# Performance work log

Hardware: AMD Instinct MI355X
Metric: run time of the kernel (lower is better)

The kernel has to match this reference:

```python
import jax, jax.numpy as jnp
import numpy as np

B, S, DIM = 4, 2048, 512
HEADS, DHEAD = 8, 64
INNER = HEADS * DHEAD


def setup_inputs() -> dict:
    key = jax.random.key(0)
    k1, k2, k3, k4 = jax.random.split(key, 4)
    x = jax.random.normal(k1, (B, S, DIM), dtype=jnp.float32)
    W_qkv = jax.random.normal(k2, (DIM, 3 * INNER), dtype=jnp.float32) * (DIM ** -0.5)
    W_out = jax.random.normal(k3, (INNER, DIM), dtype=jnp.float32) * (INNER ** -0.5)
    b_out = jnp.zeros((DIM,), dtype=jnp.float32)
    # learnable log-temperature, initialized to log(dim_head**-0.5)
    log_temp = jnp.asarray(np.log(DHEAD ** -0.5), dtype=jnp.float32)
    return {"x": x, "W_qkv": W_qkv, "log_temp": log_temp, "W_out": W_out, "b_out": b_out}


def reference(x, W_qkv, log_temp, W_out, b_out):
    b, s, _ = x.shape
    qkv = x @ W_qkv  # [b, s, 3*inner]
    q, k, v = jnp.split(qkv, 3, axis=-1)
    # [b, s, inner] -> [b, h, s, d]
    reshape = lambda t: t.reshape(b, s, HEADS, DHEAD).transpose(0, 2, 1, 3)
    q, k, v = reshape(q), reshape(k), reshape(v)
    dots = jnp.einsum("bhid,bhjd->bhij", q, k) * jnp.exp(log_temp)
    mask_value = -jnp.finfo(dots.dtype).max
    eye = jnp.eye(s, dtype=bool)
    dots = jnp.where(eye, mask_value, dots)
    attn = jax.nn.softmax(dots, axis=-1)
    out = jnp.einsum("bhij,bhjd->bhid", attn, v)
    out = out.transpose(0, 2, 1, 3).reshape(b, s, INNER)
    return out @ W_out + b_out
```

## Files before the change

kernel.cpp:

```cpp
#include <hip/hip_runtime.h>
#include <hip/hip_bf16.h>

#define BB 4
#define SS 2048
#define DIMM 512
#define HH 8
#define DD 64
#define NQKV 1536

typedef float  floatx4 __attribute__((ext_vector_type(4)));
typedef short  bf16x8  __attribute__((ext_vector_type(8)));
typedef short  bf16x4  __attribute__((ext_vector_type(4)));

#define MFMA16(A, B, C) __builtin_amdgcn_mfma_f32_16x16x32_bf16(A, B, C, 0, 0, 0)

__device__ __forceinline__ floatx4 MFMA16K16(bf16x4 a, bf16x4 b, floatx4 c) {
#if __has_builtin(__builtin_amdgcn_mfma_f32_16x16x16bf16_1k)
    return __builtin_amdgcn_mfma_f32_16x16x16bf16_1k(a, b, c, 0, 0, 0);
#else
    floatx4 d;
    asm volatile("v_mfma_f32_16x16x16_bf16 %0, %1, %2, %3"
                 : "=v"(d) : "v"(a), "v"(b), "v"(c));
    return d;
#endif
}

__device__ __forceinline__ unsigned short f2bf(float f) {
    unsigned int u = __float_as_uint(f);
    u += 0x7FFFu + ((u >> 16) & 1u);
    return (unsigned short)(u >> 16);
}

__device__ __forceinline__ unsigned int f2bf_pk(float lo, float hi) {
    float2 f; f.x = lo; f.y = hi;
    __hip_bfloat162 h = __float22bfloat162_rn(f);
    return *reinterpret_cast<unsigned int*>(&h);
}

__device__ __forceinline__ float fast_exp2(float x) {
#if __has_builtin(__builtin_amdgcn_exp2f)
    return __builtin_amdgcn_exp2f(x);
#else
    return __exp2f(x);
#endif
}

__device__ __forceinline__ void gl_lds16(const void* g, void* l) {
    __builtin_amdgcn_global_load_lds(
        (__attribute__((address_space(1))) void*)g,
        (__attribute__((address_space(3))) void*)l,
        16, 0, 0);
}

__global__ __launch_bounds__(256) void k_prep(
    const float* __restrict__ x, const float* __restrict__ W_qkv,
    const float* __restrict__ W_out,
    unsigned short* __restrict__ xb, unsigned short* __restrict__ Wq_t,
    unsigned short* __restrict__ Wo_t) {
    __shared__ float t[32][33];
    int bid = blockIdx.x, tid = threadIdx.x;
    if (bid < 4096) {
        int i = (bid * 256 + tid) * 4;
        float4 v = *(const float4*)(x + i);
        ushort4 o;
        o.x = f2bf(v.x); o.y = f2bf(v.y); o.z = f2bf(v.z); o.w = f2bf(v.w);
        *(ushort4*)(xb + i) = o;
        return;
    }
    const float* in; unsigned short* out; int R = 512, C, bx, by;
    if (bid < 4864) { in = W_qkv; out = Wq_t; C = 1536; int blk = bid - 4096; bx = blk % 48; by = blk / 48; }
    else            { in = W_out; out = Wo_t; C = 512;  int blk = bid - 4864; bx = blk % 16; by = blk / 16; }
    int tx = tid & 31, ty = tid >> 5;
    int c0 = bx * 32, r0 = by * 32;
    for (int i = 0; i < 4; i++) {
        int r = r0 + ty + i * 8;
        t[ty + i * 8][tx] = in[(size_t)r * C + c0 + tx];
    }
    __syncthreads();
    for (int i = 0; i < 4; i++) {
        int cc = c0 + ty + i * 8;
        out[(size_t)cc * R + r0 + tx] = f2bf(t[tx][ty + i * 8]);
    }
}

__global__ __launch_bounds__(256) void k_gemm_qkv(
    const unsigned short* __restrict__ A,
    const unsigned short* __restrict__ Bt,
    const float* __restrict__ log_temp,
    unsigned short* __restrict__ Qb,
    unsigned short* __restrict__ Kb,
    unsigned short* __restrict__ Vt) {
    __shared__ unsigned short smem[2][128 * 64];
    unsigned short* As = smem[0];
    unsigned short* Bs = smem[1];
    const int K = 512;
    int m0 = blockIdx.x * 128, n0 = blockIdx.y * 128;
    int tid = threadIdx.x;
    int w = tid >> 6, lane = tid & 63;
    int c = lane & 15, q4 = lane >> 4;
    int wm = w >> 1, wn = w & 1;
    float qscale = __expf(log_temp[0]) * 1.44269504f;

    floatx4 acc[4][4] = {};

    for (int k0 = 0; k0 < K; k0 += 64) {
        __syncthreads();
        for (int i = 0; i < 4; i++) {
            int cidx = w * 256 + i * 64 + lane;
            int row = cidx >> 3, cc = cidx & 7;
            int gcc = cc ^ (row & 7);
            gl_lds16(A + (size_t)(m0 + row) * K + k0 + gcc * 8,
                     As + (size_t)(w * 256 + i * 64) * 8);
            gl_lds16(Bt + (size_t)(n0 + row) * K + k0 + gcc * 8,
                     Bs + (size_t)(w * 256 + i * 64) * 8);
        }
        __syncthreads();
        bf16x8 aF[2][4], bF[2][4];
        for (int kh = 0; kh < 2; kh++)
            for (int mt = 0; mt < 4; mt++) {
                int row = wm * 64 + mt * 16 + c;
                aF[kh][mt] = *(const bf16x8*)&As[row * 64 + (((kh * 4 + q4) ^ (row & 7)) * 8)];
            }
        for (int kh = 0; kh < 2; kh++)
            for (int nt = 0; nt < 4; nt++) {
                int row = wn * 64 + nt * 16 + c;
                bF[kh][nt] = *(const bf16x8*)&Bs[row * 64 + (((kh * 4 + q4) ^ (row & 7)) * 8)];
            }
        for (int kh = 0; kh < 2; kh++)
            for (int mt = 0; mt < 4; mt++)
                for (int nt = 0; nt < 4; nt++)
                    acc[mt][nt] = MFMA16(aF[kh][mt], bF[kh][nt], acc[mt][nt]);
    }

    if (n0 < 1024) {
        for (int nt = 0; nt < 4; nt++) {
            int n = n0 + wn * 64 + nt * 16 + c;
            int t = n >> 9, inner = n & 511;
            int h = inner >> 6, d = inner & 63;
            for (int mt = 0; mt < 4; mt++) {
                for (int r = 0; r < 4; r++) {
                    int m = m0 + wm * 64 + mt * 16 + q4 * 4 + r;
                    int b = m >> 11, s = m & 2047;
                    int bh = b * 8 + h;
                    float v = acc[mt][nt][r];
                    if (t == 0)  Qb[((size_t)bh * SS + s) * 64 + d] = f2bf(v * qscale);
                    else         Kb[((size_t)bh * SS + s) * 64 + d] = f2bf(v);
                }
            }
        }
    } else {
        unsigned short* T = &smem[0][0];
        int b = m0 >> 11, s_base = m0 & 2047;
        for (int half = 0; half < 2; half++) {
            __syncthreads();
            if (wn == half) {
                for (int nt = 0; nt < 4; nt++)
                    for (int mt = 0; mt < 4; mt++)
                        for (int r = 0; r < 4; r++)
                            T[(nt * 16 + c) * 136 + wm * 64 + mt * 16 + q4 * 4 + r] =
                                f2bf(acc[mt][nt][r]);
            }
            __syncthreads();
            for (int rr = 0; rr < 4; rr++) {
                int nl = w * 16 + rr * 4 + q4;
                int ml = c * 8;
                bf16x8 v = *(const bf16x8*)&T[nl * 136 + ml];
                int n = n0 + half * 64 + nl;
                int h = (n >> 6) - 16, d = n & 63;
                int bh = b * 8 + h;
                *(bf16x8*)(Vt + ((size_t)bh * 64 + d) * SS + s_base + ml) = v;
            }
        }
    }
}

__global__ __launch_bounds__(256, 4) void k_attn(
    const unsigned short* __restrict__ Qb,
    const unsigned short* __restrict__ Kb,
    const unsigned short* __restrict__ Vt,
    unsigned short* __restrict__ AO) {
    __shared__ unsigned short Ks[2][64 * 64];
    __shared__ unsigned short Vs[2][64 * 64];
    int q0 = blockIdx.x * 128;
    int h = blockIdx.y, b = blockIdx.z;
    int bh = b * 8 + h;
    int tid = threadIdx.x, w = tid >> 6, lane = tid & 63;
    int c = lane & 15, q4 = lane >> 4;

    const unsigned short* Kbase = Kb + (size_t)bh * SS * 64;
    const unsigned short* Vbase = Vt + (size_t)bh * 64 * SS;

    bf16x8 qf[2][2];
    for (int mi = 0; mi < 2; mi++) {
        const unsigned short* qp = Qb + ((size_t)bh * SS + q0 + w * 32 + mi * 16 + c) * 64;
        qf[mi][0] = *(const bf16x8*)(qp + q4 * 8);
        qf[mi][1] = *(const bf16x8*)(qp + 32 + q4 * 8);
    }

    const unsigned short* ksrc[2];
    const unsigned short* vsrc[2];
    for (int i = 0; i < 2; i++) {
        int cidx = i * 256 + tid;
        int grow = cidx >> 3, gcc = (cidx & 7) ^ (grow & 7);
        ksrc[i] = Kbase + (size_t)grow * 64 + gcc * 8;
        vsrc[i] = Vbase + (size_t)grow * SS + gcc * 8;
    }

    for (int i = 0; i < 2; i++) {
        gl_lds16(ksrc[i], Ks[0] + (i * 256 + w * 64) * 8);
        gl_lds16(vsrc[i], Vs[0] + (i * 256 + w * 64) * 8);
    }

    int mask_j0 = (q0 + w * 32) & ~63;
    int mglob0 = q0 + w * 32 + c;
    int mglob1 = mglob0 + 16;
    floatx4 oacc[2][4] = {};
    float psum0 = 0.f, psum1 = 0.f;

    for (int j0 = 0; j0 < SS; j0 += 64) {
        int buf = (j0 >> 6) & 1;
        __syncthreads();
        if (j0 + 64 < SS) {
            for (int i = 0; i < 2; i++) {
                gl_lds16(ksrc[i] + (size_t)(j0 + 64) * 64, Ks[buf ^ 1] + (i * 256 + w * 64) * 8);
                gl_lds16(vsrc[i] + (j0 + 64), Vs[buf ^ 1] + (i * 256 + w * 64) * 8);
            }
        }
        bool diag = (j0 == mask_j0);

        for (int jt = 0; jt < 4; jt++) {
            int row = jt * 16 + c;
            bf16x8 kf0 = *(const bf16x8*)&Ks[buf][row * 64 + ((q4 ^ (row & 7)) * 8)];
            bf16x8 kf1 = *(const bf16x8*)&Ks[buf][row * 64 + (((4 + q4) ^ (row & 7)) * 8)];
            floatx4 sa0 = {}, sa1 = {};
            sa0 = MFMA16(kf0, qf[0][0], sa0);
            sa0 = MFMA16(kf1, qf[0][1], sa0);
            sa1 = MFMA16(kf0, qf[1][0], sa1);
            sa1 = MFMA16(kf1, qf[1][1], sa1);

            if (diag) {
                for (int r = 0; r < 4; r++) {
                    int jg = j0 + jt * 16 + q4 * 4 + r;
                    if (jg == mglob0) sa0[r] = -1e30f;
                    if (jg == mglob1) sa1[r] = -1e30f;
                }
            }

            float e0 = fast_exp2(sa0[0]), e1 = fast_exp2(sa0[1]);
            float e2 = fast_exp2(sa0[2]), e3 = fast_exp2(sa0[3]);
            psum0 += (e0 + e1) + (e2 + e3);
            union { bf16x4 v; unsigned int u[2]; } P0;
            P0.u[0] = f2bf_pk(e0, e1); P0.u[1] = f2bf_pk(e2, e3);
            float f0 = fast_exp2(sa1[0]), f1 = fast_exp2(sa1[1]);
            float f2 = fast_exp2(sa1[2]), f3 = fast_exp2(sa1[3]);
            psum1 += (f0 + f1) + (f2 + f3);
            union { bf16x4 v; unsigned int u[2]; } P1;
            P1.u[0] = f2bf_pk(f0, f1); P1.u[1] = f2bf_pk(f2, f3);

            int chunk = jt * 2 + (q4 >> 1);
            int sub = (q4 & 1) * 4;
            for (int dt = 0; dt < 4; dt++) {
                int vrow = dt * 16 + c;
                bf16x4 vf = *(const bf16x4*)&Vs[buf][vrow * 64 + ((chunk ^ (vrow & 7)) * 8) + sub];
                oacc[0][dt] = MFMA16K16(P0.v, vf, oacc[0][dt]);
                oacc[1][dt] = MFMA16K16(P1.v, vf, oacc[1][dt]);
            }
        }
    }

    for (int mi = 0; mi < 2; mi++) {
        float l = (mi == 0) ? psum0 : psum1;
        l += __shfl_xor(l, 16);
        l += __shfl_xor(l, 32);
        for (int r = 0; r < 4; r++) {
            float lr = __shfl(l, q4 * 4 + r, 64);
            float inv = 1.0f / lr;
            int s = q0 + w * 32 + mi * 16 + q4 * 4 + r;
            for (int dt = 0; dt < 4; dt++)
                AO[((size_t)b * SS + s) * 512 + h * 64 + dt * 16 + c] =
                    f2bf(oacc[mi][dt][r] * inv);
        }
    }
}

__global__ __launch_bounds__(256) void k_gemm_out(
    const unsigned short* __restrict__ A,
    const unsigned short* __restrict__ Bt,
    const float* __restrict__ bias,
    float* __restrict__ out) {
    __shared__ unsigned short As[128 * 64];
    __shared__ unsigned short Bs[128 * 64];
    const int K = 512;
    int m0 = blockIdx.x * 128, n0 = blockIdx.y * 128;
    int tid = threadIdx.x;
    int w = tid >> 6, lane = tid & 63;
    int c = lane & 15, q4 = lane >> 4;
    int wm = w >> 1, wn = w & 1;

    floatx4 acc[4][4] = {};

    for (int k0 = 0; k0 < K; k0 += 64) {
        __syncthreads();
        for (int i = 0; i < 4; i++) {
            int cidx = w * 256 + i * 64 + lane;
            int row = cidx >> 3, cc = cidx & 7;
            int gcc = cc ^ (row & 7);
            gl_lds16(A + (size_t)(m0 + row) * K + k0 + gcc * 8,
                     As + (size_t)(w * 256 + i * 64) * 8);
            gl_lds16(Bt + (size_t)(n0 + row) * K + k0 + gcc * 8,
                     Bs + (size_t)(w * 256 + i * 64) * 8);
        }
        __syncthreads();
        bf16x8 aF[2][4], bF[2][4];
        for (int kh = 0; kh < 2; kh++)
            for (int mt = 0; mt < 4; mt++) {
                int row = wm * 64 + mt * 16 + c;
                aF[kh][mt] = *(const bf16x8*)&As[row * 64 + (((kh * 4 + q4) ^ (row & 7)) * 8)];
            }
        for (int kh = 0; kh < 2; kh++)
            for (int nt = 0; nt < 4; nt++) {
                int row = wn * 64 + nt * 16 + c;
                bF[kh][nt] = *(const bf16x8*)&Bs[row * 64 + (((kh * 4 + q4) ^ (row & 7)) * 8)];
            }
        for (int kh = 0; kh < 2; kh++)
            for (int mt = 0; mt < 4; mt++)
                for (int nt = 0; nt < 4; nt++)
                    acc[mt][nt] = MFMA16(aF[kh][mt], bF[kh][nt], acc[mt][nt]);
    }

    for (int nt = 0; nt < 4; nt++) {
        int n = n0 + wn * 64 + nt * 16 + c;
        float bv = bias[n];
        for (int mt = 0; mt < 4; mt++) {
            for (int r = 0; r < 4; r++) {
                int m = m0 + wm * 64 + mt * 16 + q4 * 4 + r;
                out[(size_t)m * 512 + n] = acc[mt][nt][r] + bv;
            }
        }
    }
}

extern "C" void kernel_launch(void* const* d_in, const int* in_sizes, int n_in,
                              void* d_out, int out_size, void* d_ws, size_t ws_size,
                              hipStream_t stream) {
    const float* x        = (const float*)d_in[0];
    const float* W_qkv    = (const float*)d_in[1];
    const float* log_temp = (const float*)d_in[2];
    const float* W_out    = (const float*)d_in[3];
    const float* b_out    = (const float*)d_in[4];
    float* out = (float*)d_out;

    char* ws = (char*)d_ws;
    unsigned short* xb   = (unsigned short*)(ws + 0);
    unsigned short* Wq_t = (unsigned short*)(ws + 8388608);
    unsigned short* Wo_t = (unsigned short*)(ws + 9961472);
    unsigned short* Qb   = (unsigned short*)(ws + 10485760);
    unsigned short* Kb   = (unsigned short*)(ws + 18874368);
    unsigned short* Vt   = (unsigned short*)(ws + 27262976);
    unsigned short* AO   = (unsigned short*)(ws + 35651584);

    k_prep<<<5120, 256, 0, stream>>>(x, W_qkv, W_out, xb, Wq_t, Wo_t);
    k_gemm_qkv<<<dim3(64, 12), 256, 0, stream>>>(xb, Wq_t, log_temp, Qb, Kb, Vt);
    k_attn<<<dim3(16, 8, 4), 256, 0, stream>>>(Qb, Kb, Vt, AO);
    k_gemm_out<<<dim3(64, 4), 256, 0, stream>>>(AO, Wo_t, b_out, out);
}
```

Baseline: 167.9 us.

## Split attention rows across 8 waves and halve output GEMM M-tile

The attention kernel now runs 512 threads per block, and each wave owns 16 query rows instead of 32. Each thread issues a single K/V staging load per tile, so more waves share each K/V tile in LDS and latency hiding improves. The output projection GEMM switches to 64x128 tiles with one 16-row strip per wave, doubling the grid to 512 blocks to fill more CUs. The cost is less register reuse per wave, since each K fragment now feeds only one Q tile, and more B-tile traffic per output.

New measurement: 164.6 us. 1.02x faster.

```diff
diff --git a/kernel.cpp b/kernel.cpp
--- a/kernel.cpp
+++ b/kernel.cpp
@@ -174,7 +174,7 @@
     }
 }
 
-__global__ __launch_bounds__(256, 4) void k_attn(
+__global__ __launch_bounds__(512, 4) void k_attn(
     const unsigned short* __restrict__ Qb,
     const unsigned short* __restrict__ Kb,
     const unsigned short* __restrict__ Vt,
@@ -190,41 +190,33 @@
     const unsigned short* Kbase = Kb + (size_t)bh * SS * 64;
     const unsigned short* Vbase = Vt + (size_t)bh * 64 * SS;
 
-    bf16x8 qf[2][2];
-    for (int mi = 0; mi < 2; mi++) {
-        const unsigned short* qp = Qb + ((size_t)bh * SS + q0 + w * 32 + mi * 16 + c) * 64;
-        qf[mi][0] = *(const bf16x8*)(qp + q4 * 8);
-        qf[mi][1] = *(const bf16x8*)(qp + 32 + q4 * 8);
-    }
-
-    const unsigned short* ksrc[2];
-    const unsigned short* vsrc[2];
-    for (int i = 0; i < 2; i++) {
-        int cidx = i * 256 + tid;
-        int grow = cidx >> 3, gcc = (cidx & 7) ^ (grow & 7);
-        ksrc[i] = Kbase + (size_t)grow * 64 + gcc * 8;
-        vsrc[i] = Vbase + (size_t)grow * SS + gcc * 8;
-    }
-
-    for (int i = 0; i < 2; i++) {
-        gl_lds16(ksrc[i], Ks[0] + (i * 256 + w * 64) * 8);
-        gl_lds16(vsrc[i], Vs[0] + (i * 256 + w * 64) * 8);
-    }
-
-    int mask_j0 = (q0 + w * 32) & ~63;
-    int mglob0 = q0 + w * 32 + c;
-    int mglob1 = mglob0 + 16;
-    floatx4 oacc[2][4] = {};
-    float psum0 = 0.f, psum1 = 0.f;
+    bf16x8 qf[2];
+    {
+        const unsigned short* qp = Qb + ((size_t)bh * SS + q0 + w * 16 + c) * 64;
+        qf[0] = *(const bf16x8*)(qp + q4 * 8);
+        qf[1] = *(const bf16x8*)(qp + 32 + q4 * 8);
+    }
+
+    int grow = tid >> 3, gcc = (tid & 7) ^ (grow & 7);
+    const unsigned short* ksrc = Kbase + (size_t)grow * 64 + gcc * 8;
+    const unsigned short* vsrc = Vbase + (size_t)grow * SS + gcc * 8;
+    unsigned short* kdst = (unsigned short*)Ks[0] + w * 512;
+    unsigned short* vdst = (unsigned short*)Vs[0] + w * 512;
+
+    gl_lds16(ksrc, kdst);
+    gl_lds16(vsrc, vdst);
+
+    int mask_j0 = (q0 + w * 16) & ~63;
+    int mglob = q0 + w * 16 + c;
+    floatx4 oacc[4] = {};
+    float psum = 0.f;
 
     for (int j0 = 0; j0 < SS; j0 += 64) {
         int buf = (j0 >> 6) & 1;
         __syncthreads();
         if (j0 + 64 < SS) {
-            for (int i = 0; i < 2; i++) {
-                gl_lds16(ksrc[i] + (size_t)(j0 + 64) * 64, Ks[buf ^ 1] + (i * 256 + w * 64) * 8);
-                gl_lds16(vsrc[i] + (j0 + 64), Vs[buf ^ 1] + (i * 256 + w * 64) * 8);
-            }
+            gl_lds16(ksrc + (size_t)(j0 + 64) * 64, kdst + (buf ^ 1) * 4096);
+            gl_lds16(vsrc + (j0 + 64), vdst + (buf ^ 1) * 4096);
         }
         bool diag = (j0 == mask_j0);
 
@@ -232,54 +224,43 @@
             int row = jt * 16 + c;
             bf16x8 kf0 = *(const bf16x8*)&Ks[buf][row * 64 + ((q4 ^ (row & 7)) * 8)];
             bf16x8 kf1 = *(const bf16x8*)&Ks[buf][row * 64 + (((4 + q4) ^ (row & 7)) * 8)];
-            floatx4 sa0 = {}, sa1 = {};
-            sa0 = MFMA16(kf0, qf[0][0], sa0);
-            sa0 = MFMA16(kf1, qf[0][1], sa0);
-            sa1 = MFMA16(kf0, qf[1][0], sa1);
-            sa1 = MFMA16(kf1, qf[1][1], sa1);
+            floatx4 sa = {};
+            sa = MFMA16(kf0, qf[0], sa);
+            sa = MFMA16(kf1, qf[1], sa);
 
             if (diag) {
                 for (int r = 0; r < 4; r++) {
                     int jg = j0 + jt * 16 + q4 * 4 + r;
-                    if (jg == mglob0) sa0[r] = -1e30f;
-                    if (jg == mglob1) sa1[r] = -1e30f;
+                    if (jg == mglob) sa[r] = -1e30f;
                 }
             }
 
-            float e0 = fast_exp2(sa0[0]), e1 = fast_exp2(sa0[1]);
-            float e2 = fast_exp2(sa0[2]), e3 = fast_exp2(sa0[3]);
-            psum0 += (e0 + e1) + (e2 + e3);
-            union { bf16x4 v; unsigned int u[2]; } P0;
-            P0.u[0] = f2bf_pk(e0, e1); P0.u[1] = f2bf_pk(e2, e3);
-            float f0 = fast_exp2(sa1[0]), f1 = fast_exp2(sa1[1]);
-            float f2 = fast_exp2(sa1[2]), f3 = fast_exp2(sa1[3]);
-            psum1 += (f0 + f1) + (f2 + f3);
-            union { bf16x4 v; unsigned int u[2]; } P1;
-            P1.u[0] = f2bf_pk(f0, f1); P1.u[1] = f2bf_pk(f2, f3);
+            float e0 = fast_exp2(sa[0]), e1 = fast_exp2(sa[1]);
+            float e2 = fast_exp2(sa[2]), e3 = fast_exp2(sa[3]);
+            psum += (e0 + e1) + (e2 + e3);
+            union { bf16x4 v; unsigned int u[2]; } P;
+            P.u[0] = f2bf_pk(e0, e1); P.u[1] = f2bf_pk(e2, e3);
 
             int chunk = jt * 2 + (q4 >> 1);
             int sub = (q4 & 1) * 4;
             for (int dt = 0; dt < 4; dt++) {
                 int vrow = dt * 16 + c;
                 bf16x4 vf = *(const bf16x4*)&Vs[buf][vrow * 64 + ((chunk ^ (vrow & 7)) * 8) + sub];
-                oacc[0][dt] = MFMA16K16(P0.v, vf, oacc[0][dt]);
-                oacc[1][dt] = MFMA16K16(P1.v, vf, oacc[1][dt]);
-            }
-        }
-    }
-
-    for (int mi = 0; mi < 2; mi++) {
-        float l = (mi == 0) ? psum0 : psum1;
-        l += __shfl_xor(l, 16);
-        l += __shfl_xor(l, 32);
-        for (int r = 0; r < 4; r++) {
-            float lr = __shfl(l, q4 * 4 + r, 64);
-            float inv = 1.0f / lr;
-            int s = q0 + w * 32 + mi * 16 + q4 * 4 + r;
-            for (int dt = 0; dt < 4; dt++)
-                AO[((size_t)b * SS + s) * 512 + h * 64 + dt * 16 + c] =
-                    f2bf(oacc[mi][dt][r] * inv);
-        }
+                oacc[dt] = MFMA16K16(P.v, vf, oacc[dt]);
+            }
+        }
+    }
+
+    float l = psum;
+    l += __shfl_xor(l, 16);
+    l += __shfl_xor(l, 32);
+    for (int r = 0; r < 4; r++) {
+        float lr = __shfl(l, q4 * 4 + r, 64);
+        float inv = 1.0f / lr;
+        int s = q0 + w * 16 + q4 * 4 + r;
+        for (int dt = 0; dt < 4; dt++)
+            AO[((size_t)b * SS + s) * 512 + h * 64 + dt * 16 + c] =
+                f2bf(oacc[dt][r] * inv);
     }
 }
 
@@ -288,54 +269,54 @@
     const unsigned short* __restrict__ Bt,
     const float* __restrict__ bias,
     float* __restrict__ out) {
-    __shared__ unsigned short As[128 * 64];
+    __shared__ unsigned short As[64 * 64];
     __shared__ unsigned short Bs[128 * 64];
     const int K = 512;
-    int m0 = blockIdx.x * 128, n0 = blockIdx.y * 128;
+    int m0 = blockIdx.x * 64, n0 = blockIdx.y * 128;
     int tid = threadIdx.x;
     int w = tid >> 6, lane = tid & 63;
     int c = lane & 15, q4 = lane >> 4;
-    int wm = w >> 1, wn = w & 1;
-
-    floatx4 acc[4][4] = {};
+
+    floatx4 acc[8] = {};
 
     for (int k0 = 0; k0 < K; k0 += 64) {
         __syncthreads();
-        for (int i = 0; i < 4; i++) {
-            int cidx = w * 256 + i * 64 + lane;
+        for (int i = 0; i < 2; i++) {
+            int cidx = i * 256 + tid;
             int row = cidx >> 3, cc = cidx & 7;
             int gcc = cc ^ (row & 7);
             gl_lds16(A + (size_t)(m0 + row) * K + k0 + gcc * 8,
-                     As + (size_t)(w * 256 + i * 64) * 8);
+                     As + (size_t)(i * 256 + w * 64) * 8);
+        }
+        for (int i = 0; i < 4; i++) {
+            int cidx = i * 256 + tid;
+            int row = cidx >> 3, cc = cidx & 7;
+            int gcc = cc ^ (row & 7);
             gl_lds16(Bt + (size_t)(n0 + row) * K + k0 + gcc * 8,
-                     Bs + (size_t)(w * 256 + i * 64) * 8);
-        }
-        __syncthreads();
-        bf16x8 aF[2][4], bF[2][4];
-        for (int kh = 0; kh < 2; kh++)
-            for (int mt = 0; mt < 4; mt++) {
-                int row = wm * 64 + mt * 16 + c;
-                aF[kh][mt] = *(const bf16x8*)&As[row * 64 + (((kh * 4 + q4) ^ (row & 7)) * 8)];
-            }
-        for (int kh = 0; kh < 2; kh++)
-            for (int nt = 0; nt < 4; nt++) {
-                int row = wn * 64 + nt * 16 + c;
+                     Bs + (size_t)(i * 256 + w * 64) * 8);
+        }
+        __syncthreads();
+        bf16x8 aF[2], bF[2][8];
+        for (int kh = 0; kh < 2; kh++) {
+            int row = w * 16 + c;
+            aF[kh] = *(const bf16x8*)&As[row * 64 + (((kh * 4 + q4) ^ (row & 7)) * 8)];
+        }
+        for (int kh = 0; kh < 2; kh++)
+            for (int nt = 0; nt < 8; nt++) {
+                int row = nt * 16 + c;
                 bF[kh][nt] = *(const bf16x8*)&Bs[row * 64 + (((kh * 4 + q4) ^ (row & 7)) * 8)];
             }
         for (int kh = 0; kh < 2; kh++)
-            for (int mt = 0; mt < 4; mt++)
-                for (int nt = 0; nt < 4; nt++)
-                    acc[mt][nt] = MFMA16(aF[kh][mt], bF[kh][nt], acc[mt][nt]);
-    }
-
-    for (int nt = 0; nt < 4; nt++) {
-        int n = n0 + wn * 64 + nt * 16 + c;
+            for (int nt = 0; nt < 8; nt++)
+                acc[nt] = MFMA16(aF[kh], bF[kh][nt], acc[nt]);
+    }
+
+    for (int nt = 0; nt < 8; nt++) {
+        int n = n0 + nt * 16 + c;
         float bv = bias[n];
-        for (int mt = 0; mt < 4; mt++) {
-            for (int r = 0; r < 4; r++) {
-                int m = m0 + wm * 64 + mt * 16 + q4 * 4 + r;
-                out[(size_t)m * 512 + n] = acc[mt][nt][r] + bv;
-            }
+        for (int r = 0; r < 4; r++) {
+            int m = m0 + w * 16 + q4 * 4 + r;
+            out[(size_t)m * 512 + n] = acc[nt][r] + bv;
         }
     }
 }
@@ -361,6 +342,6 @@
 
     k_prep<<<5120, 256, 0, stream>>>(x, W_qkv, W_out, xb, Wq_t, Wo_t);
     k_gemm_qkv<<<dim3(64, 12), 256, 0, stream>>>(xb, Wq_t, log_temp, Qb, Kb, Vt);
-    k_attn<<<dim3(16, 8, 4), 256, 0, stream>>>(Qb, Kb, Vt, AO);
-    k_gemm_out<<<dim3(64, 4), 256, 0, stream>>>(AO, Wo_t, b_out, out);
-}
+    k_attn<<<dim3(16, 8, 4), 512, 0, stream>>>(Qb, Kb, Vt, AO);
+    k_gemm_out<<<dim3(128, 4), 256, 0, stream>>>(AO, Wo_t, b_out, out);
+}
```
